# Kernel optimization log

Measured on AMD Instinct MI355X. Metric: run time of the kernel, lower is better.

## Reference

```python
import jax, jax.numpy as jnp
import numpy as np

H, D, BS = 32, 128, 64          # num_heads, head_dim, gate block_size
GATE_DIM = 64
GATE_TEMP = 2.0                 # _GATE_TARGET_TEMPERATURE
CLAMP_MIN, CLAMP_MAX = -50.0, 50.0


def _rotate_half(x):
    x1, x2 = jnp.split(x, 2, axis=-1)
    return jnp.concatenate([-x2, x1], axis=-1)


def setup_inputs() -> dict:
    key = jax.random.key(0)
    ks = jax.random.split(key, 8)
    B, S, E = 1, 2048, 4096
    hidden_states = jax.random.normal(ks[0], (B, S, E), jnp.float32) * 0.02
    # standard RoPE tables, [B, S, D]
    inv_freq = 1.0 / (10000.0 ** (jnp.arange(0, D, 2, dtype=jnp.float32) / D))
    freqs = jnp.arange(S, dtype=jnp.float32)[:, None] * inv_freq[None, :]
    emb = jnp.concatenate([freqs, freqs], axis=-1)
    cos = jnp.broadcast_to(jnp.cos(emb)[None], (B, S, D)).astype(jnp.float32)
    sin = jnp.broadcast_to(jnp.sin(emb)[None], (B, S, D)).astype(jnp.float32)
    Wq = jax.random.normal(ks[1], (E, E), jnp.float32) * 0.02
    Wk = jax.random.normal(ks[2], (E, E), jnp.float32) * 0.02
    Wv = jax.random.normal(ks[3], (E, E), jnp.float32) * 0.02
    Wo = jax.random.normal(ks[4], (E, E), jnp.float32) * 0.02
    Wg_q = jax.random.normal(ks[5], (GATE_DIM, D), jnp.float32) * 0.05
    Wg_k = jax.random.normal(ks[6], (GATE_DIM, D), jnp.float32) * 0.05
    return {"hidden_states": hidden_states, "cos": cos, "sin": sin,
            "Wq": Wq, "Wk": Wk, "Wv": Wv, "Wo": Wo,
            "Wg_q": Wg_q, "Wg_k": Wg_k}


def reference(hidden_states, cos, sin, Wq, Wk, Wv, Wo, Wg_q, Wg_k):
    B, S, E = hidden_states.shape
    scale = np.float32(1.0 / np.sqrt(D))

    # ---- base attention (training path: full dense attention w/ scores) ----
    q = (hidden_states @ Wq.T).reshape(B, S, H, D).transpose(0, 2, 1, 3)  # [B,H,S,D]
    k = (hidden_states @ Wk.T).reshape(B, S, H, D).transpose(0, 2, 1, 3)
    v = (hidden_states @ Wv.T).reshape(B, S, H, D).transpose(0, 2, 1, 3)

    # _apply_rotary_pos_emb: cos/sin are 3D [B,S,D] -> unsqueeze head dim
    c, s = cos[:, None], sin[:, None]
    q = q * c + _rotate_half(q) * s
    k = k * c + _rotate_half(k) * s

    scores = jnp.einsum('bhqd,bhkd->bhqk', q, k) * scale  # [B,H,S,S]
    causal = jnp.tril(jnp.ones((S, S), dtype=bool))
    scores = jnp.where(causal, scores, -jnp.inf)
    attn = jax.nn.softmax(scores, axis=-1)
    ctx = jnp.einsum('bhqk,bhkd->bhqd', attn, v)
    attn_output = ctx.transpose(0, 2, 1, 3).reshape(B, S, E) @ Wo.T

    # ---- _compute_gate_target: blockwise maxpool -> clamp -> tempered softmax ----
    NB = S // BS  # S divisible by BS, so the -inf padding branch is a no-op
    block_max = scores.reshape(B, H, NB, BS, NB, BS).max(axis=(3, 5))  # [B,H,NB,NB]
    finite = jnp.isfinite(block_max)
    block_max = jnp.where(finite, jnp.clip(block_max, CLAMP_MIN, CLAMP_MAX), block_max)
    gate_target = jax.nn.softmax(
        block_max.reshape(B, H, NB * NB) / GATE_TEMP, axis=-1
    ).reshape(B, H, NB, NB)

    # ---- AttnGate prediction: mean-pooled block Q/K -> low-rank block logits ----
    qb = q.reshape(B, H, NB, BS, D).mean(axis=3)  # [B,H,NB,D]
    kb = k.reshape(B, H, NB, BS, D).mean(axis=3)
    gq = jnp.einsum('bhnd,gd->bhng', qb, Wg_q)
    gk = jnp.einsum('bhnd,gd->bhng', kb, Wg_k)
    glogits = jnp.einsum('bhqg,bhkg->bhqk', gq, gk) * np.float32(1.0 / np.sqrt(GATE_DIM))
    bmask = jnp.tril(jnp.ones((NB, NB), dtype=bool))  # block-causal
    glogits = jnp.where(bmask, glogits, -jnp.inf)
    gate_pred = jax.nn.softmax(
        glogits.reshape(B, H, NB * NB), axis=-1
    ).reshape(B, H, NB, NB)

    return attn_output, gate_pred, gate_target
```

## Files before the change

kernel.cpp:

```cpp
#include <hip/hip_runtime.h>
#include <stdint.h>

#define S_LEN 2048
#define EMB   4096
#define NHEAD 32
#define DHEAD 128
#define NBLK  32
#define GDIM  64

typedef float  f32x4  __attribute__((ext_vector_type(4)));
typedef __bf16 bf16x8 __attribute__((ext_vector_type(8)));
typedef unsigned short u16;

__device__ __forceinline__ u16 f2bf(float f) {
  uint32_t u = __float_as_uint(f);
  u += 0x7fffu + ((u >> 16) & 1u);
  return (u16)(u >> 16);
}
__device__ __forceinline__ float bf2f(u16 u) {
  return __uint_as_float(((uint32_t)u) << 16);
}

__device__ __forceinline__ void ld_lds16(const u16* g, u16* l) {
  __builtin_amdgcn_global_load_lds((const __attribute__((address_space(1))) void*)g,
                                   (__attribute__((address_space(3))) void*)l, 16, 0, 0);
}

__global__ void conv_f32_bf16(const float* __restrict__ in, u16* __restrict__ out, int n4) {
  int i = blockIdx.x * 256 + threadIdx.x;
  if (i >= n4) return;
  float4 v = ((const float4*)in)[i];
  ushort4 o;
  o.x = f2bf(v.x); o.y = f2bf(v.y); o.z = f2bf(v.z); o.w = f2bf(v.w);
  ((ushort4*)out)[i] = o;
}

__global__ void conv3_f32_bf16(const float* __restrict__ a, const float* __restrict__ b,
                               const float* __restrict__ c, u16* __restrict__ oa,
                               u16* __restrict__ ob, u16* __restrict__ oc, int n4) {
  int i = blockIdx.x * 256 + threadIdx.x;
  if (i >= n4) return;
  const float* in = (blockIdx.y == 0) ? a : (blockIdx.y == 1) ? b : c;
  u16* out = (blockIdx.y == 0) ? oa : (blockIdx.y == 1) ? ob : oc;
  float4 v = ((const float4*)in)[i];
  ushort4 o;
  o.x = f2bf(v.x); o.y = f2bf(v.y); o.z = f2bf(v.z); o.w = f2bf(v.w);
  ((ushort4*)out)[i] = o;
}

__global__ void __launch_bounds__(256, 2) qkv_gemm(
    const u16* __restrict__ A, const u16* __restrict__ Bq, const u16* __restrict__ Bk,
    const u16* __restrict__ Bv, u16* __restrict__ outq, u16* __restrict__ outk,
    u16* __restrict__ outvt, const float* __restrict__ cosp, const float* __restrict__ sinp)
{
  __shared__ u16 lA[128 * 32];
  __shared__ u16 lB[128 * 32];
  __shared__ u16 lT[128 * 132];

  const int tid = threadIdx.x;
  const int w = tid >> 6, lane = tid & 63;
  const int r = lane & 15, qd = lane >> 4;
  const int nb = blockIdx.x;
  const int which = nb >> 5;
  const int h = nb & 31;
  const int m0 = blockIdx.y * 128, n0 = h * 128;
  const int K = EMB;
  const u16* B = (which == 0) ? Bq : (which == 1) ? Bk : Bv;

  f32x4 acc[2][8];
#pragma unroll
  for (int mi = 0; mi < 2; ++mi)
#pragma unroll
    for (int ni = 0; ni < 8; ++ni) acc[mi][ni] = (f32x4){0.f, 0.f, 0.f, 0.f};

  const u16* Ab = A + (size_t)(m0 + w * 16 + (lane >> 2)) * K + (lane & 3) * 8;
  const u16* Bb = B + (size_t)(n0 + w * 16 + (lane >> 2)) * K + (lane & 3) * 8;
  u16* lAb = &lA[(w * 16) * 32];
  u16* lBb = &lB[(w * 16) * 32];

  for (int k0 = 0; k0 < K; k0 += 32) {
    __syncthreads();
    ld_lds16(Ab + k0, lAb);
    ld_lds16(Ab + (size_t)64 * K + k0, lAb + 64 * 32);
    ld_lds16(Bb + k0, lBb);
    ld_lds16(Bb + (size_t)64 * K + k0, lBb + 64 * 32);
    __syncthreads();
    bf16x8 af0 = *(const bf16x8*)&lA[(w * 32 + r) * 32 + qd * 8];
    bf16x8 af1 = *(const bf16x8*)&lA[(w * 32 + 16 + r) * 32 + qd * 8];
#pragma unroll
    for (int ni = 0; ni < 8; ++ni) {
      bf16x8 bf = *(const bf16x8*)&lB[(ni * 16 + r) * 32 + qd * 8];
      acc[0][ni] = __builtin_amdgcn_mfma_f32_16x16x32_bf16(af0, bf, acc[0][ni], 0, 0, 0);
      acc[1][ni] = __builtin_amdgcn_mfma_f32_16x16x32_bf16(af1, bf, acc[1][ni], 0, 0, 0);
    }
  }

  if (which < 2) {
    u16* out = which ? outk : outq;
#pragma unroll
    for (int mi = 0; mi < 2; ++mi)
#pragma unroll
      for (int ni = 0; ni < 4; ++ni)
#pragma unroll
        for (int rg = 0; rg < 4; ++rg) {
          int srow = m0 + w * 32 + mi * 16 + qd * 4 + rg;
          int dlo = ni * 16 + r;
          float c = cosp[srow * DHEAD + dlo];
          float s = sinp[srow * DHEAD + dlo];
          float lo = acc[mi][ni][rg], hi = acc[mi][ni + 4][rg];
          size_t base = ((size_t)h * S_LEN + srow) * DHEAD;
          out[base + dlo]      = f2bf(lo * c - hi * s);
          out[base + dlo + 64] = f2bf(hi * c + lo * s);
        }
  } else {
#pragma unroll
    for (int mi = 0; mi < 2; ++mi)
#pragma unroll
      for (int ni = 0; ni < 8; ++ni)
#pragma unroll
        for (int rg = 0; rg < 4; ++rg) {
          int sl = w * 32 + mi * 16 + qd * 4 + rg;
          lT[sl * 132 + ni * 16 + r] = f2bf(acc[mi][ni][rg]);
        }
    __syncthreads();
    const int d = tid >> 1, sh = (tid & 1) * 64;
    size_t obase = ((size_t)h * DHEAD + d) * S_LEN + m0 + sh;
#pragma unroll
    for (int i8 = 0; i8 < 8; ++i8) {
      u16 tmp[8];
#pragma unroll
      for (int j = 0; j < 8; ++j) tmp[j] = lT[(sh + i8 * 8 + j) * 132 + d];
      *(uint4*)&outvt[obase + i8 * 8] = *(uint4*)tmp;
    }
  }
}

__global__ void __launch_bounds__(256, 2) gemm_out(
    const u16* __restrict__ A, const u16* __restrict__ B, float* __restrict__ out)
{
  __shared__ u16 lA[128 * 32];
  __shared__ u16 lB[128 * 32];
  const int tid = threadIdx.x;
  const int w = tid >> 6, lane = tid & 63;
  const int r = lane & 15, qd = lane >> 4;
  const int m0 = blockIdx.y * 128, n0 = blockIdx.x * 128;
  const int K = EMB;

  f32x4 acc[2][8];
#pragma unroll
  for (int mi = 0; mi < 2; ++mi)
#pragma unroll
    for (int ni = 0; ni < 8; ++ni) acc[mi][ni] = (f32x4){0.f, 0.f, 0.f, 0.f};

  const u16* Ab = A + (size_t)(m0 + w * 16 + (lane >> 2)) * K + (lane & 3) * 8;
  const u16* Bb = B + (size_t)(n0 + w * 16 + (lane >> 2)) * K + (lane & 3) * 8;
  u16* lAb = &lA[(w * 16) * 32];
  u16* lBb = &lB[(w * 16) * 32];

  for (int k0 = 0; k0 < K; k0 += 32) {
    __syncthreads();
    ld_lds16(Ab + k0, lAb);
    ld_lds16(Ab + (size_t)64 * K + k0, lAb + 64 * 32);
    ld_lds16(Bb + k0, lBb);
    ld_lds16(Bb + (size_t)64 * K + k0, lBb + 64 * 32);
    __syncthreads();
    bf16x8 af0 = *(const bf16x8*)&lA[(w * 32 + r) * 32 + qd * 8];
    bf16x8 af1 = *(const bf16x8*)&lA[(w * 32 + 16 + r) * 32 + qd * 8];
#pragma unroll
    for (int ni = 0; ni < 8; ++ni) {
      bf16x8 bf = *(const bf16x8*)&lB[(ni * 16 + r) * 32 + qd * 8];
      acc[0][ni] = __builtin_amdgcn_mfma_f32_16x16x32_bf16(af0, bf, acc[0][ni], 0, 0, 0);
      acc[1][ni] = __builtin_amdgcn_mfma_f32_16x16x32_bf16(af1, bf, acc[1][ni], 0, 0, 0);
    }
  }
#pragma unroll
  for (int mi = 0; mi < 2; ++mi)
#pragma unroll
    for (int ni = 0; ni < 8; ++ni)
#pragma unroll
      for (int rg = 0; rg < 4; ++rg) {
        int srow = m0 + w * 32 + mi * 16 + qd * 4 + rg;
        out[(size_t)srow * EMB + n0 + ni * 16 + r] = acc[mi][ni][rg];
      }
}

__global__ void __launch_bounds__(256, 2) attn_fwd(
    const u16* __restrict__ qg, const u16* __restrict__ kg, const u16* __restrict__ vtg,
    u16* __restrict__ ctx, float* __restrict__ bmax)
{
  __shared__ u16 lK[64 * 132];
  __shared__ u16 lV[128 * 76];
  __shared__ u16 lP[64 * 76];
  __shared__ float lBM[4 * NBLK];

  const int tid = threadIdx.x;
  const int w = tid >> 6, lane = tid & 63;
  const int r = lane & 15, qd = lane >> 4;
  const int h = blockIdx.y;
  const u16* ksrc = kg + (size_t)h * S_LEN * DHEAD;
  const u16* vsrc = vtg + (size_t)h * DHEAD * S_LEN;
  const float scale = 0.08838834764831845f;

  for (int qsel = 0; qsel < 2; ++qsel) {
    const int qb = qsel ? (31 - (int)blockIdx.x) : (int)blockIdx.x;

    bf16x8 qf[4];
    {
      const u16* qp = qg + ((size_t)h * S_LEN + qb * 64 + w * 16 + r) * DHEAD + qd * 8;
#pragma unroll
      for (int ki = 0; ki < 4; ++ki) qf[ki] = *(const bf16x8*)(qp + ki * 32);
    }

    f32x4 o[8];
#pragma unroll
    for (int dt = 0; dt < 8; ++dt) o[dt] = (f32x4){0.f, 0.f, 0.f, 0.f};
    float m_run[4], l_run[4];
#pragma unroll
    for (int rg = 0; rg < 4; ++rg) { m_run[rg] = -__builtin_inff(); l_run[rg] = 0.f; }

    for (int kb = 0; kb <= qb; ++kb) {
      __syncthreads();
#pragma unroll
      for (int i = 0; i < 4; ++i) {
        int c = tid + 256 * i;
        int row = c >> 4, col = (c & 15) * 8;
        *(uint4*)&lK[row * 132 + col] = *(const uint4*)(ksrc + (size_t)(kb * 64 + row) * DHEAD + col);
      }
#pragma unroll
      for (int i = 0; i < 4; ++i) {
        int c = tid + 256 * i;
        int row = c >> 3, col = (c & 7) * 8;
        *(uint4*)&lV[row * 76 + col] = *(const uint4*)(vsrc + (size_t)row * S_LEN + kb * 64 + col);
      }
      __syncthreads();

      f32x4 sf[4];
#pragma unroll
      for (int nt = 0; nt < 4; ++nt) sf[nt] = (f32x4){0.f, 0.f, 0.f, 0.f};
#pragma unroll
      for (int ki = 0; ki < 4; ++ki)
#pragma unroll
        for (int nt = 0; nt < 4; ++nt) {
          bf16x8 bf = *(const bf16x8*)&lK[(nt * 16 + r) * 132 + ki * 32 + qd * 8];
          sf[nt] = __builtin_amdgcn_mfma_f32_16x16x32_bf16(qf[ki], bf, sf[nt], 0, 0, 0);
        }

      float rmax[4];
#pragma unroll
      for (int rg = 0; rg < 4; ++rg) rmax[rg] = -__builtin_inff();
#pragma unroll
      for (int nt = 0; nt < 4; ++nt)
#pragma unroll
        for (int rg = 0; rg < 4; ++rg) {
          float s = sf[nt][rg] * scale;
          if (kb == qb) {
            int col = nt * 16 + r, row = w * 16 + qd * 4 + rg;
            if (col > row) s = -__builtin_inff();
          }
          sf[nt][rg] = s;
          rmax[rg] = fmaxf(rmax[rg], s);
        }
#pragma unroll
      for (int rg = 0; rg < 4; ++rg) {
        float v = rmax[rg];
        v = fmaxf(v, __shfl_xor(v, 1));
        v = fmaxf(v, __shfl_xor(v, 2));
        v = fmaxf(v, __shfl_xor(v, 4));
        v = fmaxf(v, __shfl_xor(v, 8));
        rmax[rg] = v;
      }
      {
        float v = fmaxf(fmaxf(rmax[0], rmax[1]), fmaxf(rmax[2], rmax[3]));
        v = fmaxf(v, __shfl_xor(v, 16));
        v = fmaxf(v, __shfl_xor(v, 32));
        if (lane == 0) lBM[w * NBLK + kb] = v;
      }

      float alpha[4], rsum[4];
#pragma unroll
      for (int rg = 0; rg < 4; ++rg) {
        float mn = fmaxf(m_run[rg], rmax[rg]);
        alpha[rg] = __expf(m_run[rg] - mn);
        m_run[rg] = mn;
        rsum[rg] = 0.f;
      }
#pragma unroll
      for (int nt = 0; nt < 4; ++nt)
#pragma unroll
        for (int rg = 0; rg < 4; ++rg) {
          float p = __expf(sf[nt][rg] - m_run[rg]);
          sf[nt][rg] = p;
          rsum[rg] += p;
        }
#pragma unroll
      for (int rg = 0; rg < 4; ++rg) {
        float v = rsum[rg];
        v += __shfl_xor(v, 1);
        v += __shfl_xor(v, 2);
        v += __shfl_xor(v, 4);
        v += __shfl_xor(v, 8);
        l_run[rg] = l_run[rg] * alpha[rg] + v;
      }
#pragma unroll
      for (int nt = 0; nt < 4; ++nt)
#pragma unroll
        for (int rg = 0; rg < 4; ++rg)
          lP[(w * 16 + qd * 4 + rg) * 76 + nt * 16 + r] = f2bf(sf[nt][rg]);
#pragma unroll
      for (int dt = 0; dt < 8; ++dt)
#pragma unroll
        for (int rg = 0; rg < 4; ++rg) o[dt][rg] *= alpha[rg];
      bf16x8 pa0 = *(const bf16x8*)&lP[(w * 16 + r) * 76 + qd * 8];
      bf16x8 pa1 = *(const bf16x8*)&lP[(w * 16 + r) * 76 + 32 + qd * 8];
#pragma unroll
      for (int dt = 0; dt < 8; ++dt) {
        bf16x8 bv0 = *(const bf16x8*)&lV[(dt * 16 + r) * 76 + qd * 8];
        bf16x8 bv1 = *(const bf16x8*)&lV[(dt * 16 + r) * 76 + 32 + qd * 8];
        o[dt] = __builtin_amdgcn_mfma_f32_16x16x32_bf16(pa0, bv0, o[dt], 0, 0, 0);
        o[dt] = __builtin_amdgcn_mfma_f32_16x16x32_bf16(pa1, bv1, o[dt], 0, 0, 0);
      }
    }

    float inv[4];
#pragma unroll
    for (int rg = 0; rg < 4; ++rg) inv[rg] = 1.f / l_run[rg];
#pragma unroll
    for (int dt = 0; dt < 8; ++dt)
#pragma unroll
      for (int rg = 0; rg < 4; ++rg) {
        int srow = qb * 64 + w * 16 + qd * 4 + rg;
        ctx[(size_t)srow * EMB + h * DHEAD + dt * 16 + r] = f2bf(o[dt][rg] * inv[rg]);
      }
    __syncthreads();
    if (tid <= qb) {
      float v = fmaxf(fmaxf(lBM[0 * NBLK + tid], lBM[1 * NBLK + tid]),
                      fmaxf(lBM[2 * NBLK + tid], lBM[3 * NBLK + tid]));
      bmax[((size_t)h * NBLK + qb) * NBLK + tid] = v;
    }
  }
}

__global__ void bmean2(const u16* __restrict__ q, const u16* __restrict__ k,
                       float* __restrict__ qo, float* __restrict__ ko) {
  int nb = blockIdx.x, h = blockIdx.y, t = threadIdx.x;
  const u16* x = blockIdx.z ? k : q;
  float* out = blockIdx.z ? ko : qo;
  const u16* p = x + ((size_t)h * S_LEN + nb * 64) * DHEAD + t * 2;
  float s0 = 0.f, s1 = 0.f;
#pragma unroll 8
  for (int i = 0; i < 64; ++i) {
    uint32_t v = *(const uint32_t*)(p + (size_t)i * DHEAD);
    s0 += bf2f((u16)v);
    s1 += bf2f((u16)(v >> 16));
  }
  float2 rr = {s0 * (1.f / 64.f), s1 * (1.f / 64.f)};
  *(float2*)&out[((size_t)h * NBLK + nb) * DHEAD + t * 2] = rr;
}

__global__ void __launch_bounds__(256) gate_kernel(
    const float* __restrict__ qm, const float* __restrict__ km,
    const float* __restrict__ Wgq, const float* __restrict__ Wgk,
    const float* __restrict__ bmx, float* __restrict__ gpred, float* __restrict__ gtgt)
{
  __shared__ float gq[NBLK * GDIM], gk[NBLK * GDIM];
  __shared__ float red[256];
  const int h = blockIdx.x, tid = threadIdx.x;

  for (int i = 0; i < 8; ++i) {
    int e = tid + 256 * i;
    int n = e >> 6, g = e & 63;
    const float* qrow = qm + ((size_t)h * NBLK + n) * DHEAD;
    const float* krow = km + ((size_t)h * NBLK + n) * DHEAD;
    const float* wq = Wgq + g * DHEAD;
    const float* wk = Wgk + g * DHEAD;
    float s1 = 0.f, s2 = 0.f;
    for (int d = 0; d < DHEAD; ++d) { s1 += qrow[d] * wq[d]; s2 += krow[d] * wk[d]; }
    gq[e] = s1; gk[e] = s2;
  }
  __syncthreads();

  float gl[4];
  for (int i = 0; i < 4; ++i) {
    int idx = tid + 256 * i;
    int qn = idx >> 5, kn = idx & 31;
    if (kn <= qn) {
      float s = 0.f;
      for (int g = 0; g < GDIM; ++g) s += gq[qn * GDIM + g] * gk[kn * GDIM + g];
      gl[i] = s * 0.125f;
    } else gl[i] = -__builtin_inff();
  }
  float mx = fmaxf(fmaxf(gl[0], gl[1]), fmaxf(gl[2], gl[3]));
  red[tid] = mx; __syncthreads();
  for (int st = 128; st > 0; st >>= 1) { if (tid < st) red[tid] = fmaxf(red[tid], red[tid + st]); __syncthreads(); }
  float gmax = red[0]; __syncthreads();
  float ex[4], lsum = 0.f;
  for (int i = 0; i < 4; ++i) { ex[i] = __expf(gl[i] - gmax); lsum += ex[i]; }
  red[tid] = lsum; __syncthreads();
  for (int st = 128; st > 0; st >>= 1) { if (tid < st) red[tid] += red[tid + st]; __syncthreads(); }
  float invs = 1.f / red[0]; __syncthreads();
  for (int i = 0; i < 4; ++i) gpred[(size_t)h * 1024 + tid + 256 * i] = ex[i] * invs;

  float tl[4];
  for (int i = 0; i < 4; ++i) {
    int idx = tid + 256 * i;
    int qn = idx >> 5, kn = idx & 31;
    tl[i] = (kn <= qn) ? fminf(fmaxf(bmx[(size_t)h * 1024 + idx], -50.f), 50.f) * 0.5f
                       : -__builtin_inff();
  }
  float mx2 = fmaxf(fmaxf(tl[0], tl[1]), fmaxf(tl[2], tl[3]));
  red[tid] = mx2; __syncthreads();
  for (int st = 128; st > 0; st >>= 1) { if (tid < st) red[tid] = fmaxf(red[tid], red[tid + st]); __syncthreads(); }
  float tmax = red[0]; __syncthreads();
  float ex2[4], ls2 = 0.f;
  for (int i = 0; i < 4; ++i) { ex2[i] = __expf(tl[i] - tmax); ls2 += ex2[i]; }
  red[tid] = ls2; __syncthreads();
  for (int st = 128; st > 0; st >>= 1) { if (tid < st) red[tid] += red[tid + st]; __syncthreads(); }
  float inv2 = 1.f / red[0];
  for (int i = 0; i < 4; ++i) gtgt[(size_t)h * 1024 + tid + 256 * i] = ex2[i] * inv2;
}

extern "C" void kernel_launch(void* const* d_in, const int* in_sizes, int n_in,
                              void* d_out, int out_size, void* d_ws, size_t ws_size,
                              hipStream_t stream) {
  const float* hidden = (const float*)d_in[0];
  const float* cosp   = (const float*)d_in[1];
  const float* sinp   = (const float*)d_in[2];
  const float* Wq     = (const float*)d_in[3];
  const float* Wk     = (const float*)d_in[4];
  const float* Wv     = (const float*)d_in[5];
  const float* Wo     = (const float*)d_in[6];
  const float* Wgq    = (const float*)d_in[7];
  const float* Wgk    = (const float*)d_in[8];

  char* ws = (char*)d_ws;
  u16* wqb = (u16*)ws;
  u16* wkb = (u16*)(ws + 33554432);
  u16* hid = (u16*)(ws + 67108864);
  u16* qbf = (u16*)(ws + 83886080);
  u16* kbf = (u16*)(ws + 100663296);
  u16* vtb = (u16*)(ws + 117440512);
  float* bmx = (float*)(ws + 33554432);
  float* qmn = (float*)(ws + 33554432 + 131072);
  float* kmn = (float*)(ws + 33554432 + 655360);
  u16* ctx = hid;
  u16* wvb = (u16*)d_out;

  float* attn_out = (float*)d_out;
  float* gpred = attn_out + (size_t)S_LEN * EMB;
  float* gtgt  = gpred + NHEAD * NBLK * NBLK;

  conv3_f32_bf16<<<dim3(16384, 3), 256, 0, stream>>>(Wq, Wk, Wv, wqb, wkb, wvb, 4194304);
  conv_f32_bf16<<<8192, 256, 0, stream>>>(hidden, hid, 2097152);

  qkv_gemm<<<dim3(96, 16), 256, 0, stream>>>(hid, wqb, wkb, wvb, qbf, kbf, vtb, cosp, sinp);

  conv_f32_bf16<<<16384, 256, 0, stream>>>(Wo, wqb, 4194304);

  attn_fwd<<<dim3(16, NHEAD), 256, 0, stream>>>(qbf, kbf, vtb, ctx, bmx);

  bmean2<<<dim3(NBLK, NHEAD, 2), 128, 0, stream>>>(qbf, kbf, qmn, kmn);
  gate_kernel<<<NHEAD, 256, 0, stream>>>(qmn, kmn, Wgq, Wgk, bmx, gpred, gtgt);

  gemm_out<<<dim3(32, 16), 256, 0, stream>>>(ctx, wqb, attn_out);
}
```

Before: 791.2 us.

## Rewrite QKV GEMM with 256x256 tiles, 4-stage LDS pipeline and swizzle

Replaces the 128x128 QKV GEMM with a 512-thread 256x256 tile kernel that streams A/B through a 4-deep LDS ring with explicit vmcnt waits, staging loads interleaved with MFMA groups. LDS is XOR-swizzled to reduce bank conflicts and s_setprio raises MFMA priority. The larger tile raises arithmetic intensity and the pipeline hides global load latency. In exchange it uses 128KB of dynamic LDS and many accumulators, which limits occupancy, and the grid shrinks to 384 blocks, which may under-fill the CUs.

Result: faster. 770.6 us (-2.6%).

```diff
diff --git a/kernel.cpp b/kernel.cpp
--- a/kernel.cpp
+++ b/kernel.cpp
@@ -48,89 +48,157 @@
   ((ushort4*)out)[i] = o;
 }
 
-__global__ void __launch_bounds__(256, 2) qkv_gemm(
+__global__ void __launch_bounds__(512, 2) qkv_gemm_256(
     const u16* __restrict__ A, const u16* __restrict__ Bq, const u16* __restrict__ Bk,
     const u16* __restrict__ Bv, u16* __restrict__ outq, u16* __restrict__ outk,
     u16* __restrict__ outvt, const float* __restrict__ cosp, const float* __restrict__ sinp)
 {
-  __shared__ u16 lA[128 * 32];
-  __shared__ u16 lB[128 * 32];
-  __shared__ u16 lT[128 * 132];
-
-  const int tid = threadIdx.x;
-  const int w = tid >> 6, lane = tid & 63;
-  const int r = lane & 15, qd = lane >> 4;
-  const int nb = blockIdx.x;
-  const int which = nb >> 5;
-  const int h = nb & 31;
-  const int m0 = blockIdx.y * 128, n0 = h * 128;
-  const int K = EMB;
+  extern __shared__ u16 lds[];
+
+  const int tid  = threadIdx.x;
+  const int w    = tid >> 6;
+  const int lane = tid & 63;
+  const int r    = lane & 15;
+  const int qd   = lane >> 4;
+  const int wr   = w >> 2;
+  const int wc   = w & 3;
+
+  const int which = blockIdx.x >> 4;
+  const int nt    = blockIdx.x & 15;
+  const int m0    = blockIdx.y * 256;
+  const int n0    = nt * 256;
+  const int K     = EMB;
   const u16* B = (which == 0) ? Bq : (which == 1) ? Bk : Bv;
 
-  f32x4 acc[2][8];
-#pragma unroll
-  for (int mi = 0; mi < 2; ++mi)
-#pragma unroll
-    for (int ni = 0; ni < 8; ++ni) acc[mi][ni] = (f32x4){0.f, 0.f, 0.f, 0.f};
-
-  const u16* Ab = A + (size_t)(m0 + w * 16 + (lane >> 2)) * K + (lane & 3) * 8;
-  const u16* Bb = B + (size_t)(n0 + w * 16 + (lane >> 2)) * K + (lane & 3) * 8;
-  u16* lAb = &lA[(w * 16) * 32];
-  u16* lBb = &lB[(w * 16) * 32];
-
-  for (int k0 = 0; k0 < K; k0 += 32) {
-    __syncthreads();
-    ld_lds16(Ab + k0, lAb);
-    ld_lds16(Ab + (size_t)64 * K + k0, lAb + 64 * 32);
-    ld_lds16(Bb + k0, lBb);
-    ld_lds16(Bb + (size_t)64 * K + k0, lBb + 64 * 32);
-    __syncthreads();
-    bf16x8 af0 = *(const bf16x8*)&lA[(w * 32 + r) * 32 + qd * 8];
-    bf16x8 af1 = *(const bf16x8*)&lA[(w * 32 + 16 + r) * 32 + qd * 8];
-#pragma unroll
-    for (int ni = 0; ni < 8; ++ni) {
-      bf16x8 bf = *(const bf16x8*)&lB[(ni * 16 + r) * 32 + qd * 8];
-      acc[0][ni] = __builtin_amdgcn_mfma_f32_16x16x32_bf16(af0, bf, acc[0][ni], 0, 0, 0);
-      acc[1][ni] = __builtin_amdgcn_mfma_f32_16x16x32_bf16(af1, bf, acc[1][ni], 0, 0, 0);
-    }
+  const int cb0 = (wc >> 1) * 128 + (wc & 1) * 32;
+  const int cb1 = cb0 + 16;
+  const int cb2 = cb0 + 64;
+  const int cb3 = cb0 + 80;
+
+  const int fragoff = r * 32 + ((qd ^ ((r >> 1) & 3)) << 3);
+
+  const int srow_st = w * 16 + (lane >> 2);
+  const int sslot   = ((lane & 3) ^ ((lane >> 3) & 3)) * 8;
+  const u16* Ab0 = A + (size_t)(m0 + srow_st) * K + sslot;
+  const u16* Ab1 = Ab0 + (size_t)128 * K;
+  const u16* Bb0 = B + (size_t)(n0 + srow_st) * K + sslot;
+  const u16* Bb1 = Bb0 + (size_t)128 * K;
+
+  f32x4 acc[8][4];
+#pragma unroll
+  for (int mi = 0; mi < 8; ++mi)
+#pragma unroll
+    for (int ni = 0; ni < 4; ++ni) acc[mi][ni] = (f32x4){0.f, 0.f, 0.f, 0.f};
+
+  auto stageA = [&](int tt) {
+    u16* d = lds + (tt & 3) * 8192 + w * 512;
+    const int kk = tt * 32;
+    ld_lds16(Ab0 + kk, d);
+    ld_lds16(Ab1 + kk, d + 4096);
+  };
+  auto stageB = [&](int tt) {
+    u16* d = lds + 32768 + (tt & 3) * 8192 + w * 512;
+    const int kk = tt * 32;
+    ld_lds16(Bb0 + kk, d);
+    ld_lds16(Bb1 + kk, d + 4096);
+  };
+
+  stageA(0); stageB(0);
+  stageA(1); stageB(1);
+  stageA(2); stageB(2);
+
+  for (int t = 0; t < 128; ++t) {
+    const int buf = t & 3;
+    if (t < 126)       asm volatile("s_waitcnt vmcnt(8) lgkmcnt(0)" ::: "memory");
+    else if (t == 126) asm volatile("s_waitcnt vmcnt(4) lgkmcnt(0)" ::: "memory");
+    else               asm volatile("s_waitcnt vmcnt(0) lgkmcnt(0)" ::: "memory");
+    __builtin_amdgcn_sched_barrier(0);
+    __builtin_amdgcn_s_barrier();
+
+    const u16* lAb = lds + buf * 8192 + wr * 128 * 32;
+    const u16* lBb = lds + 32768 + buf * 8192;
+
+    bf16x8 bfr[4];
+    bfr[0] = *(const bf16x8*)(lBb + cb0 * 32 + fragoff);
+    bfr[1] = *(const bf16x8*)(lBb + cb1 * 32 + fragoff);
+    bfr[2] = *(const bf16x8*)(lBb + cb2 * 32 + fragoff);
+    bfr[3] = *(const bf16x8*)(lBb + cb3 * 32 + fragoff);
+
+    bf16x8 af[4];
+#pragma unroll
+    for (int mi = 0; mi < 4; ++mi) af[mi] = *(const bf16x8*)(lAb + mi * 512 + fragoff);
+    if (t < 125) stageA(t + 3);
+
+    __builtin_amdgcn_s_setprio(1);
+#pragma unroll
+    for (int mi = 0; mi < 4; ++mi)
+#pragma unroll
+      for (int ni = 0; ni < 4; ++ni)
+        acc[mi][ni] = __builtin_amdgcn_mfma_f32_16x16x32_bf16(af[mi], bfr[ni], acc[mi][ni], 0, 0, 0);
+    __builtin_amdgcn_s_setprio(0);
+
+    bf16x8 af2[4];
+#pragma unroll
+    for (int mi = 0; mi < 4; ++mi) af2[mi] = *(const bf16x8*)(lAb + (mi + 4) * 512 + fragoff);
+    if (t < 125) stageB(t + 3);
+
+    __builtin_amdgcn_s_setprio(1);
+#pragma unroll
+    for (int mi = 0; mi < 4; ++mi)
+#pragma unroll
+      for (int ni = 0; ni < 4; ++ni)
+        acc[mi + 4][ni] = __builtin_amdgcn_mfma_f32_16x16x32_bf16(af2[mi], bfr[ni], acc[mi + 4][ni], 0, 0, 0);
+    __builtin_amdgcn_s_setprio(0);
   }
 
   if (which < 2) {
     u16* out = which ? outk : outq;
-#pragma unroll
-    for (int mi = 0; mi < 2; ++mi)
-#pragma unroll
-      for (int ni = 0; ni < 4; ++ni)
+    const int hh = 2 * nt + (wc >> 1);
+    const int dbase = (wc & 1) * 32;
+#pragma unroll
+    for (int mi = 0; mi < 8; ++mi)
+#pragma unroll
+      for (int ni = 0; ni < 2; ++ni) {
+        const int dlo = dbase + ni * 16 + r;
 #pragma unroll
         for (int rg = 0; rg < 4; ++rg) {
-          int srow = m0 + w * 32 + mi * 16 + qd * 4 + rg;
-          int dlo = ni * 16 + r;
+          int srow = m0 + wr * 128 + mi * 16 + qd * 4 + rg;
           float c = cosp[srow * DHEAD + dlo];
           float s = sinp[srow * DHEAD + dlo];
-          float lo = acc[mi][ni][rg], hi = acc[mi][ni + 4][rg];
-          size_t base = ((size_t)h * S_LEN + srow) * DHEAD;
+          float lo = acc[mi][ni][rg], hi = acc[mi][ni + 2][rg];
+          size_t base = ((size_t)hh * S_LEN + srow) * DHEAD;
           out[base + dlo]      = f2bf(lo * c - hi * s);
           out[base + dlo + 64] = f2bf(hi * c + lo * s);
         }
+      }
   } else {
-#pragma unroll
-    for (int mi = 0; mi < 2; ++mi)
-#pragma unroll
-      for (int ni = 0; ni < 8; ++ni)
-#pragma unroll
-        for (int rg = 0; rg < 4; ++rg) {
-          int sl = w * 32 + mi * 16 + qd * 4 + rg;
-          lT[sl * 132 + ni * 16 + r] = f2bf(acc[mi][ni][rg]);
+    u16* lT = lds;
+#pragma unroll
+    for (int ch = 0; ch < 2; ++ch) {
+      __syncthreads();
+      if (wr == ch) {
+#pragma unroll
+        for (int mi = 0; mi < 8; ++mi) {
+          const int lr = mi * 16 + qd * 4;
+          const int cbs[4] = {cb0, cb1, cb2, cb3};
+#pragma unroll
+          for (int ni = 0; ni < 4; ++ni) {
+            const int col = cbs[ni] + r;
+#pragma unroll
+            for (int rg = 0; rg < 4; ++rg)
+              lT[col * 136 + lr + rg] = f2bf(acc[mi][ni][rg]);
+          }
         }
-    __syncthreads();
-    const int d = tid >> 1, sh = (tid & 1) * 64;
-    size_t obase = ((size_t)h * DHEAD + d) * S_LEN + m0 + sh;
-#pragma unroll
-    for (int i8 = 0; i8 < 8; ++i8) {
-      u16 tmp[8];
-#pragma unroll
-      for (int j = 0; j < 8; ++j) tmp[j] = lT[(sh + i8 * 8 + j) * 132 + d];
-      *(uint4*)&outvt[obase + i8 * 8] = *(uint4*)tmp;
+      }
+      __syncthreads();
+      const int c = tid >> 1, sh = (tid & 1) * 64;
+      const int hh2 = 2 * nt + (c >> 7), d = c & 127;
+      size_t obase = ((size_t)hh2 * DHEAD + d) * S_LEN + m0 + ch * 128 + sh;
+#pragma unroll
+      for (int i8 = 0; i8 < 8; ++i8) {
+        uint4 v = *(const uint4*)&lT[c * 136 + sh + i8 * 8];
+        *(uint4*)&outvt[obase + i8 * 8] = v;
+      }
     }
   }
 }
@@ -452,7 +520,13 @@
   conv3_f32_bf16<<<dim3(16384, 3), 256, 0, stream>>>(Wq, Wk, Wv, wqb, wkb, wvb, 4194304);
   conv_f32_bf16<<<8192, 256, 0, stream>>>(hidden, hid, 2097152);
 
-  qkv_gemm<<<dim3(96, 16), 256, 0, stream>>>(hid, wqb, wkb, wvb, qbf, kbf, vtb, cosp, sinp);
+  static bool attr_set = false;
+  if (!attr_set) {
+    (void)hipFuncSetAttribute((const void*)qkv_gemm_256,
+                              hipFuncAttributeMaxDynamicSharedMemorySize, 131072);
+    attr_set = true;
+  }
+  qkv_gemm_256<<<dim3(48, 8), 512, 131072, stream>>>(hid, wqb, wkb, wvb, qbf, kbf, vtb, cosp, sinp);
 
   conv_f32_bf16<<<16384, 256, 0, stream>>>(Wo, wqb, 4194304);
 
```
